# Optimization experiments

Measured on AMD Instinct MI355X. Metric: run time of the kernel, lower is better.

The kernel has to match this reference:

```python
import jax, jax.numpy as jnp
import numpy as np

B, S, C, H, W = 8, 64, 3, 224, 224   # batch, n_segments, channels, height, width
E, P = 128, 16                        # embed_dim, patch size of feature extractor


def _conv(x, w, b, stride, padding):
    y = jax.lax.conv_general_dilated(
        x, w, (stride, stride), padding,
        dimension_numbers=('NCHW', 'OIHW', 'NCHW'))
    return y + b[None, :, None, None]


def setup_inputs() -> dict:
    key = jax.random.key(0)
    k1, k2, k3 = jax.random.split(key, 3)
    img = jax.random.normal(k1, (B, C, H, W), jnp.float32)
    # SpixelNet stand-in: 3x3 conv -> n_segments logit channels
    w_spixel = jax.random.normal(k2, (S, C, 3, 3), jnp.float32) * 0.1
    b_spixel = jnp.zeros((S,), jnp.float32)
    # feature extractor stand-in: 16x16/16 patch conv -> embed_dim, then GAP
    w_patch = jax.random.normal(k3, (E, C, P, P), jnp.float32) * 0.02
    b_patch = jnp.zeros((E,), jnp.float32)
    return dict(img=img, w_spixel=w_spixel, b_spixel=b_spixel,
                w_patch=w_patch, b_patch=b_patch)


def reference(img, w_spixel, b_spixel, w_patch, b_patch):
    # superpixel tokenizer -> segment logits, argmax -> hard labels
    logits = _conv(img, w_spixel, b_spixel, 1, 'SAME')          # [B,S,H,W]
    labels = jnp.argmax(logits, axis=1)                          # [B,H,W] int

    # replicate per-batch torch.unique (sorted unique labels, zero-padded)
    flat = labels.reshape(B, -1)
    present = jnp.zeros((B, S), bool).at[jnp.arange(B)[:, None], flat].set(True)
    vals = jnp.where(present, jnp.arange(S)[None, :], S)
    uniq = jnp.sort(vals, axis=1)                                # uniques first
    uniq = jnp.where(uniq < S, uniq, 0)                          # pad with 0 like torch.zeros

    # broadcast-compare mask build + masked extract (the memory-bound op)
    mask = (labels[:, None, :, :] == uniq[:, :, None, None]).astype(img.dtype)  # [B,S,H,W]
    seg = (img[:, None, :, :, :] * mask[:, :, None, :, :]).reshape(B * S, C, H, W)

    # feature extractor: patch conv + global average pool
    feat = _conv(seg, w_patch, b_patch, P, 'VALID')              # [B*S,E,H/P,W/P]
    feat = feat.mean(axis=(2, 3))                                # [B*S,E]
    return feat.reshape(B, S, E)
```

## Files before the change

### kernel.cpp

```cpp
#include <hip/hip_runtime.h>

#define BD 8
#define SD 64
#define CD 3
#define HD 224
#define WD 224
#define ED 128
#define PD 16
#define HWD (HD*WD)
#define KD (CD*PD*PD)
#define PRT 8
#define CHK (HWD/PRT)

typedef float v2f __attribute__((ext_vector_type(2)));

__device__ float              g_part[BD * CD * PRT * SD * 256];
__device__ int                g_labels[BD * HWD];
__device__ unsigned long long g_ppres[BD * PRT];

__global__ __launch_bounds__(256) void k_labels(
    const float* __restrict__ img,
    const float* __restrict__ wsp,
    const float* __restrict__ bsp)
{
    __shared__ __align__(16) float w_s[(SD / 2) * 56];
    const int tid = threadIdx.x;
    #pragma unroll
    for (int t = tid; t < (SD / 2) * 56; t += 256) {
        const int q = t / 56, r = t - q * 56;
        const int j = r >> 1, s = 2 * q + (r & 1);
        w_s[t] = (j < 27) ? wsp[s * 27 + j] : bsp[s];
    }
    __syncthreads();

    const int p = blockIdx.x * 256 + tid;
    const int b = blockIdx.y;
    const int h = p / WD;
    const int w = p - h * WD;

    const float* ib = img + (size_t)b * CD * HWD;
    float pix[27];
    #pragma unroll
    for (int c = 0; c < 3; ++c)
        #pragma unroll
        for (int dh = 0; dh < 3; ++dh)
            #pragma unroll
            for (int dw = 0; dw < 3; ++dw) {
                int hh = h + dh - 1, ww = w + dw - 1;
                bool ok = (hh >= 0) & (hh < HD) & (ww >= 0) & (ww < WD);
                pix[(c * 3 + dh) * 3 + dw] = ok ? ib[c * HWD + hh * WD + ww] : 0.f;
            }

    v2f pd[27];
    #pragma unroll
    for (int j = 0; j < 27; ++j) { pd[j].x = pix[j]; pd[j].y = pix[j]; }

    float best = -INFINITY;
    int bi = 0;
    for (int q = 0; q < SD / 2; ++q) {
        const v2f* wrow = (const v2f*)w_s + q * 28;
        v2f acc = wrow[27];
        #pragma unroll
        for (int j = 0; j < 27; ++j)
            acc = __builtin_elementwise_fma(pd[j], wrow[j], acc);
        if (acc.x > best) { best = acc.x; bi = 2 * q; }
        if (acc.y > best) { best = acc.y; bi = 2 * q + 1; }
    }
    g_labels[b * HWD + p] = bi;
}

__global__ __launch_bounds__(256) void k_hist(const float* __restrict__ img)
{
    const int part = blockIdx.x, c = blockIdx.y, b = blockIdx.z;
    const int tid = threadIdx.x;

    __shared__ float acc[SD * 256];
    __shared__ unsigned long long pm;
    #pragma unroll
    for (int k = 0; k < 16; ++k)
        ((float4*)acc)[k * 256 + tid] = make_float4(0.f, 0.f, 0.f, 0.f);
    if (tid == 0) pm = 0ull;
    __syncthreads();

    const int start = part * CHK;
    const int end   = start + CHK;
    const int*   lb = g_labels + (size_t)b * HWD;
    const float* ic = img + ((size_t)b * CD + c) * HWD;

    unsigned long long m = 0ull;
    int p = start + tid;
    int   lab = (p < end) ? lb[p] : 0;
    float val = (p < end) ? ic[p] : 0.f;
    while (p < end) {
        const int pn = p + 256;
        const int   labn = (pn < end) ? lb[pn] : 0;
        const float valn = (pn < end) ? ic[pn] : 0.f;
        const int h = p / WD, w = p - h * WD;
        const int cell = ((h & 15) << 4) | (w & 15);
        atomicAdd(&acc[lab * 256 + cell], val);
        m |= 1ull << lab;
        p = pn; lab = labn; val = valn;
    }
    #pragma unroll
    for (int d = 1; d < 64; d <<= 1) m |= __shfl_xor(m, d, 64);
    if ((tid & 63) == 0) atomicOr(&pm, m);
    __syncthreads();

    float4* dst = (float4*)(g_part + (((size_t)(b * CD + c)) * PRT + part) * (SD * 256));
    #pragma unroll
    for (int k = 0; k < 16; ++k)
        dst[k * 256 + tid] = ((float4*)acc)[k * 256 + tid];
    if (c == 0 && tid == 0) g_ppres[b * PRT + part] = pm;
}

__global__ __launch_bounds__(256) void k_out(
    const float* __restrict__ wp,
    const float* __restrict__ bp,
    float* __restrict__ out)
{
    __shared__ float4 gs4[KD / 4];
    const int i = blockIdx.x;
    const int b = blockIdx.y;
    const int z = blockIdx.z;
    const int tid = threadIdx.x;
    const int lane = tid & 63;
    const int wv = tid >> 6;

    unsigned long long m = 0ull;
    #pragma unroll
    for (int p2 = 0; p2 < PRT; ++p2) m |= g_ppres[b * PRT + p2];

    int l = 0;
    if (i < __popcll(m)) {
        unsigned long long mm = m;
        for (int t = 0; t < i; ++t) mm &= mm - 1;
        l = __builtin_ctzll(mm);
    }

    if (tid < KD / 4) {
        const int c = tid >> 6, cell4 = tid & 63;
        const float4* src = (const float4*)g_part
            + ((size_t)(b * CD + c) * PRT) * 4096 + l * 64 + cell4;
        float4 s = src[0];
        #pragma unroll
        for (int p2 = 1; p2 < PRT; ++p2) {
            float4 v = src[(size_t)p2 * 4096];
            s.x += v.x; s.y += v.y; s.z += v.z; s.w += v.w;
        }
        gs4[tid] = s;
    }
    __syncthreads();

    const float4 g0 = gs4[lane], g1 = gs4[lane + 64], g2 = gs4[lane + 128];

    #pragma unroll 4
    for (int j = 0; j < 16; ++j) {
        const int e = z * 64 + wv * 16 + j;
        const float4* wr = (const float4*)(wp + (size_t)e * KD);
        float4 a0 = wr[lane], a1 = wr[lane + 64], a2 = wr[lane + 128];
        float acc = g0.x * a0.x;
        acc = fmaf(g0.y, a0.y, acc); acc = fmaf(g0.z, a0.z, acc); acc = fmaf(g0.w, a0.w, acc);
        acc = fmaf(g1.x, a1.x, acc); acc = fmaf(g1.y, a1.y, acc);
        acc = fmaf(g1.z, a1.z, acc); acc = fmaf(g1.w, a1.w, acc);
        acc = fmaf(g2.x, a2.x, acc); acc = fmaf(g2.y, a2.y, acc);
        acc = fmaf(g2.z, a2.z, acc); acc = fmaf(g2.w, a2.w, acc);
        #pragma unroll
        for (int off = 32; off; off >>= 1) acc += __shfl_xor(acc, off, 64);
        if (lane == 0)
            out[(size_t)(b * SD + i) * ED + e] = bp[e] + acc * (1.f / 196.f);
    }
}

extern "C" void kernel_launch(void* const* d_in, const int* in_sizes, int n_in,
                              void* d_out, int out_size, void* d_ws, size_t ws_size,
                              hipStream_t stream) {
    const float *img = nullptr, *wsp = nullptr, *bsp = nullptr, *wp = nullptr, *bp = nullptr;
    for (int i = 0; i < n_in; ++i) {
        switch (in_sizes[i]) {
            case BD * CD * HWD:      img = (const float*)d_in[i]; break;
            case SD * CD * 9:        wsp = (const float*)d_in[i]; break;
            case SD:                 bsp = (const float*)d_in[i]; break;
            case ED * CD * PD * PD:  wp  = (const float*)d_in[i]; break;
            case ED:                 bp  = (const float*)d_in[i]; break;
        }
    }
    float* out = (float*)d_out;

    dim3 g1(HWD / 256, BD, 1);
    k_labels<<<g1, 256, 0, stream>>>(img, wsp, bsp);

    dim3 g2(PRT, CD, BD);
    k_hist<<<g2, 256, 0, stream>>>(img);

    dim3 g3(SD, BD, 2);
    k_out<<<g3, 256, 0, stream>>>(wp, bp, out);
}
```

Baseline: 121.4 us.

## Vectorize histogram loads and batch four segments per output block

The histogram kernel now reads labels and pixels as int4/float4 groups of four adjacent pixels in a fixed unrolled loop, replacing the strided scalar loop with prefetch. The output kernel handles four segment indices per block, so each patch-weight row it loads is reused across four dot products, and the embedding dimension is split into four z-slices. This cuts global weight traffic and raises per-thread arithmetic intensity, at the cost of more registers and shared memory per block.

```diff
diff --git a/kernel.cpp b/kernel.cpp
--- a/kernel.cpp
+++ b/kernel.cpp
@@ -11,6 +11,7 @@
 #define KD (CD*PD*PD)
 #define PRT 8
 #define CHK (HWD/PRT)
+#define IG 4
 
 typedef float v2f __attribute__((ext_vector_type(2)));
 
@@ -83,24 +84,32 @@
     __syncthreads();
 
     const int start = part * CHK;
-    const int end   = start + CHK;
     const int*   lb = g_labels + (size_t)b * HWD;
     const float* ic = img + ((size_t)b * CD + c) * HWD;
 
     unsigned long long m = 0ull;
-    int p = start + tid;
-    int   lab = (p < end) ? lb[p] : 0;
-    float val = (p < end) ? ic[p] : 0.f;
-    while (p < end) {
-        const int pn = p + 256;
-        const int   labn = (pn < end) ? lb[pn] : 0;
-        const float valn = (pn < end) ? ic[pn] : 0.f;
-        const int h = p / WD, w = p - h * WD;
-        const int cell = ((h & 15) << 4) | (w & 15);
-        atomicAdd(&acc[lab * 256 + cell], val);
-        m |= 1ull << lab;
-        p = pn; lab = labn; val = valn;
-    }
+
+    #define HIST_GROUP(g)                                                  \
+    {                                                                      \
+        const int p4 = start + (g) * 4;                                    \
+        const int4   l4 = *(const int4*)(lb + p4);                         \
+        const float4 v4 = *(const float4*)(ic + p4);                       \
+        const int h = p4 / WD;                                             \
+        const int w0 = p4 - h * WD;                                        \
+        const int base = ((h & 15) << 4) | (w0 & 15);                      \
+        atomicAdd(&acc[l4.x * 256 + base + 0], v4.x);                      \
+        atomicAdd(&acc[l4.y * 256 + base + 1], v4.y);                      \
+        atomicAdd(&acc[l4.z * 256 + base + 2], v4.z);                      \
+        atomicAdd(&acc[l4.w * 256 + base + 3], v4.w);                      \
+        m |= 1ull << l4.x; m |= 1ull << l4.y;                              \
+        m |= 1ull << l4.z; m |= 1ull << l4.w;                              \
+    }
+
+    #pragma unroll
+    for (int it = 0; it < 6; ++it) HIST_GROUP(tid + it * 256);
+    if (tid < (CHK / 4 - 6 * 256)) HIST_GROUP(tid + 6 * 256);
+    #undef HIST_GROUP
+
     #pragma unroll
     for (int d = 1; d < 64; d <<= 1) m |= __shfl_xor(m, d, 64);
     if ((tid & 63) == 0) atomicOr(&pm, m);
@@ -118,8 +127,8 @@
     const float* __restrict__ bp,
     float* __restrict__ out)
 {
-    __shared__ float4 gs4[KD / 4];
-    const int i = blockIdx.x;
+    __shared__ float4 gs4[IG][KD / 4];
+    const int ig = blockIdx.x;
     const int b = blockIdx.y;
     const int z = blockIdx.z;
     const int tid = threadIdx.x;
@@ -129,45 +138,75 @@
     unsigned long long m = 0ull;
     #pragma unroll
     for (int p2 = 0; p2 < PRT; ++p2) m |= g_ppres[b * PRT + p2];
-
-    int l = 0;
-    if (i < __popcll(m)) {
-        unsigned long long mm = m;
-        for (int t = 0; t < i; ++t) mm &= mm - 1;
-        l = __builtin_ctzll(mm);
-    }
-
-    if (tid < KD / 4) {
-        const int c = tid >> 6, cell4 = tid & 63;
+    const int nu = __popcll(m);
+
+    int ls[IG];
+    #pragma unroll
+    for (int ii = 0; ii < IG; ++ii) {
+        const int i = ig * IG + ii;
+        int l = 0;
+        if (i < nu) {
+            unsigned long long mm = m;
+            for (int t = 0; t < i; ++t) mm &= mm - 1;
+            l = __builtin_ctzll(mm);
+        }
+        ls[ii] = l;
+    }
+
+    #pragma unroll
+    for (int k = 0; k < 3; ++k) {
+        const int t = tid + k * 256;
+        const int ii = t / (KD / 4 / 1) / 1;
+        const int ii_ = t / 192, idx = t - ii_ * 192;
+        (void)ii;
+        const int c = idx >> 6, cell4 = idx & 63;
         const float4* src = (const float4*)g_part
-            + ((size_t)(b * CD + c) * PRT) * 4096 + l * 64 + cell4;
+            + ((size_t)(b * CD + c) * PRT) * 4096 + ls[ii_] * 64 + cell4;
         float4 s = src[0];
         #pragma unroll
         for (int p2 = 1; p2 < PRT; ++p2) {
             float4 v = src[(size_t)p2 * 4096];
             s.x += v.x; s.y += v.y; s.z += v.z; s.w += v.w;
         }
-        gs4[tid] = s;
-    }
-    __syncthreads();
-
-    const float4 g0 = gs4[lane], g1 = gs4[lane + 64], g2 = gs4[lane + 128];
-
-    #pragma unroll 4
-    for (int j = 0; j < 16; ++j) {
-        const int e = z * 64 + wv * 16 + j;
+        gs4[ii_][idx] = s;
+    }
+    __syncthreads();
+
+    float4 G[IG][3];
+    #pragma unroll
+    for (int ii = 0; ii < IG; ++ii) {
+        G[ii][0] = gs4[ii][lane];
+        G[ii][1] = gs4[ii][lane + 64];
+        G[ii][2] = gs4[ii][lane + 128];
+    }
+
+    #pragma unroll 2
+    for (int j = 0; j < 8; ++j) {
+        const int e = z * 32 + wv * 8 + j;
         const float4* wr = (const float4*)(wp + (size_t)e * KD);
-        float4 a0 = wr[lane], a1 = wr[lane + 64], a2 = wr[lane + 128];
-        float acc = g0.x * a0.x;
-        acc = fmaf(g0.y, a0.y, acc); acc = fmaf(g0.z, a0.z, acc); acc = fmaf(g0.w, a0.w, acc);
-        acc = fmaf(g1.x, a1.x, acc); acc = fmaf(g1.y, a1.y, acc);
-        acc = fmaf(g1.z, a1.z, acc); acc = fmaf(g1.w, a1.w, acc);
-        acc = fmaf(g2.x, a2.x, acc); acc = fmaf(g2.y, a2.y, acc);
-        acc = fmaf(g2.z, a2.z, acc); acc = fmaf(g2.w, a2.w, acc);
-        #pragma unroll
-        for (int off = 32; off; off >>= 1) acc += __shfl_xor(acc, off, 64);
-        if (lane == 0)
-            out[(size_t)(b * SD + i) * ED + e] = bp[e] + acc * (1.f / 196.f);
+        const float4 a0 = wr[lane], a1 = wr[lane + 64], a2 = wr[lane + 128];
+        float acc[IG];
+        #pragma unroll
+        for (int ii = 0; ii < IG; ++ii) {
+            float t = G[ii][0].x * a0.x;
+            t = fmaf(G[ii][0].y, a0.y, t); t = fmaf(G[ii][0].z, a0.z, t);
+            t = fmaf(G[ii][0].w, a0.w, t);
+            t = fmaf(G[ii][1].x, a1.x, t); t = fmaf(G[ii][1].y, a1.y, t);
+            t = fmaf(G[ii][1].z, a1.z, t); t = fmaf(G[ii][1].w, a1.w, t);
+            t = fmaf(G[ii][2].x, a2.x, t); t = fmaf(G[ii][2].y, a2.y, t);
+            t = fmaf(G[ii][2].z, a2.z, t); t = fmaf(G[ii][2].w, a2.w, t);
+            acc[ii] = t;
+        }
+        #pragma unroll
+        for (int off = 32; off; off >>= 1) {
+            #pragma unroll
+            for (int ii = 0; ii < IG; ++ii) acc[ii] += __shfl_xor(acc[ii], off, 64);
+        }
+        if (lane == 0) {
+            #pragma unroll
+            for (int ii = 0; ii < IG; ++ii)
+                out[(size_t)(b * SD + ig * IG + ii) * ED + e] = bp[e] + acc[ii] * (1.f / 196.f);
+        }
     }
 }
 
@@ -192,6 +231,6 @@
     dim3 g2(PRT, CD, BD);
     k_hist<<<g2, 256, 0, stream>>>(img);
 
-    dim3 g3(SD, BD, 2);
+    dim3 g3(SD / IG, BD, 4);
     k_out<<<g3, 256, 0, stream>>>(wp, bp, out);
 }
```

Result: no change. 119.2 us (-1.8%).
